# Kernel optimization log

Hardware: AMD Instinct MI355X
Metric: run time of the kernel (lower is better)

## Reference

```python
import jax, jax.numpy as jnp
import numpy as np

B, W, G, E, NI, K = 2048, 8192, 8, 128, 16, 15


def setup_inputs() -> dict:
    key = jax.random.key(0)
    ks = jax.random.split(key, 12)
    wavelengths_nm = jnp.linspace(300.0, 400.0, W, dtype=jnp.float32)
    # Rayleigh optical depth (Hansen & Travis style approximation), AMF=1 column
    lam_um = wavelengths_nm / 1000.0
    rayleigh_od = (0.008569 * lam_um ** -4
                   * (1.0 + 0.0113 * lam_um ** -2 + 0.00013 * lam_um ** -4)).astype(jnp.float32)
    return {
        "gas_columns": jax.random.uniform(ks[0], (B, G), jnp.float32),
        "instrument_ids": jax.random.randint(ks[1], (B,), 0, NI),
        "nuisance_latent": jax.random.normal(ks[2], (B, G), jnp.float32),
        "air_mass": 1.0 + 2.0 * jax.random.uniform(ks[3], (B,), jnp.float32),
        "wavelengths_nm": wavelengths_nm,
        "absorption": 0.1 * jax.random.uniform(ks[4], (G, W), jnp.float32),
        "continuum_basis": 0.05 * jax.random.normal(ks[5], (G + 1, W), jnp.float32),
        "rayleigh_od": rayleigh_od,
        "embed_table": jax.random.normal(ks[6], (NI, E), jnp.float32),
        "w1": jax.random.normal(ks[7], (E + G, 64), jnp.float32) / np.sqrt(E + G),
        "b1": jnp.zeros((64,), jnp.float32),
        "w2": jax.random.normal(ks[8], (64, 7), jnp.float32) / 8.0,
        "b2": jnp.zeros((7,), jnp.float32),
    }


def _gaussian_kernel(width_px, kernel_size):
    half = (kernel_size - 1) / 2
    pos = jnp.linspace(-half, half, kernel_size, dtype=width_px.dtype)  # [K]
    k = jnp.exp(-0.5 * (pos[None, :] / (width_px[:, None] + 1e-6)) ** 2)  # [B,K]
    return k / k.sum(axis=1, keepdims=True)


def _forward(gas_columns, nuisance_latent, air_mass, wavelengths_nm, absorption,
             continuum_basis, rayleigh_od, embed_table, w1, b1, w2, b2,
             instrument_ids):
    b = gas_columns.shape[0]
    am = air_mass[:, None]                                   # [B,1]
    scaled = gas_columns * am                                # [B,G]
    optical_depth = scaled @ absorption                      # [B,W]
    ones = jnp.ones((b, 1), gas_columns.dtype)
    continuum = jnp.concatenate([gas_columns, ones], axis=1) @ continuum_basis  # [B,W]
    differential = optical_depth + continuum + am * rayleigh_od[None, :]

    # nuisance MLP on [latent, embedding]
    embed = embed_table[instrument_ids]                      # [B,E]
    nin = jnp.concatenate([nuisance_latent, embed], axis=-1)
    h = jax.nn.gelu(nin @ w1 + b1, approximate=False)
    p = h @ w2 + b2                                          # [B,7]

    gain = jax.nn.softplus(p[:, 0]) + 0.001
    offset = p[:, 1]
    woff = 0.05 * jnp.tanh(p[:, 2])
    wscale = 1.0 + 0.005 * jnp.tanh(p[:, 3])
    lsf = jnp.clip(jax.nn.softplus(p[:, 4]) + 0.001, 0.2, 5.0)
    stray = jax.nn.sigmoid(p[:, 5]) * 0.05
    nonlin = 0.02 * jnp.tanh(p[:, 6])

    # per-sample wavelength shift/scale + linear resampling
    new_wl = wavelengths_nm[None, :] * wscale[:, None] + woff[:, None]  # [B,W]
    differential = jax.vmap(lambda wq, d: jnp.interp(wq, wavelengths_nm, d))(new_wl, differential)

    # per-sample Gaussian LSF convolution (replicate padding)
    kernel = _gaussian_kernel(lsf, K)                        # [B,K]
    pad = K // 2
    padded = jnp.pad(differential, ((0, 0), (pad, pad)), mode='edge')  # [B,W+K-1]
    n = differential.shape[1]
    convolved = sum(padded[:, k:k + n] * kernel[:, k:k + 1] for k in range(K))

    counts = jnp.exp(-convolved)
    post = gain[:, None] * counts + offset[:, None]
    total_nl = jnp.clip(nonlin, -0.04, 0.04)                 # instrument nonlinearity = 0
    nl_counts = post + total_nl[:, None] * post ** 2
    total_stray = jnp.clip(stray, 0.0, 0.2)                  # instrument stray = 0
    simulated = (1.0 - total_stray[:, None]) * nl_counts \
        + total_stray[:, None] * nl_counts.mean(axis=1, keepdims=True)
    return simulated


def reference(gas_columns, instrument_ids, nuisance_latent, air_mass,
              wavelengths_nm, absorption, continuum_basis, rayleigh_od,
              embed_table, w1, b1, w2, b2):
    return _forward(gas_columns, nuisance_latent, air_mass, wavelengths_nm,
                    absorption, continuum_basis, rayleigh_od, embed_table,
                    w1, b1, w2, b2, instrument_ids)
```

## Files before the change

kernel.cpp:

```cpp
#include <hip/hip_runtime.h>

#define W_ 8192
#define NBATCH 2048
#define NT 256
#define NWAVE 4
#define SEGW 2048
#define CCH 256
#define NCHW 8
#define IRW 272

typedef unsigned short u16_t;
typedef _Float16 h2v __attribute__((ext_vector_type(2)));

__device__ __forceinline__ u16_t f2h(float x){ _Float16 h=(_Float16)x; return __builtin_bit_cast(u16_t,h); }
__device__ __forceinline__ float h2f(u16_t u){ return (float)__builtin_bit_cast(_Float16,u); }
__device__ __forceinline__ unsigned pk2(float a,float b){ return (unsigned)f2h(a)|((unsigned)f2h(b)<<16); }
__device__ __forceinline__ float dot2u(unsigned a,unsigned b,float c){
#if __has_builtin(__builtin_amdgcn_fdot2)
  return __builtin_amdgcn_fdot2(__builtin_bit_cast(h2v,a),__builtin_bit_cast(h2v,b),c,false);
#else
  h2v ha=__builtin_bit_cast(h2v,a), hb=__builtin_bit_cast(h2v,b);
  return c+(float)ha[0]*(float)hb[0]+(float)ha[1]*(float)hb[1];
#endif
}
__device__ __forceinline__ unsigned pkrtz(float a,float b){
#if __has_builtin(__builtin_amdgcn_cvt_pkrtz)
  return __builtin_bit_cast(unsigned, __builtin_amdgcn_cvt_pkrtz(a,b));
#else
  return pk2(a,b);
#endif
}
__device__ __forceinline__ unsigned alignb(unsigned hi, unsigned lo){
#if __has_builtin(__builtin_amdgcn_alignbit)
  return __builtin_amdgcn_alignbit(hi, lo, 16);
#else
  return (lo >> 16) | (hi << 16);
#endif
}
__device__ __forceinline__ float softplusf(float x){ return fmaxf(x,0.f)+log1pf(expf(-fabsf(x))); }
__device__ __forceinline__ unsigned rflv(unsigned v){
  return (unsigned)__builtin_amdgcn_readfirstlane((int)v);
}
__device__ __forceinline__ float rflvf(float v){
  return __builtin_bit_cast(float, __builtin_amdgcn_readfirstlane(__builtin_bit_cast(int, v)));
}

__global__ __launch_bounds__(256, 2)
void doas_prep4(const float* __restrict__ absn, const float* __restrict__ cbn,
                const float* __restrict__ ray, const int* __restrict__ iid,
                const float* __restrict__ nuis, const float* __restrict__ emb,
                const float* __restrict__ w1, const float* __restrict__ b1,
                const float* __restrict__ w2, const float* __restrict__ b2,
                unsigned* __restrict__ Tp, float* __restrict__ params){
  const int tid = threadIdx.x;
  const int b = blockIdx.x;
  const int wid = tid >> 6, l = tid & 63;

  if (b < 32){
    const int w = b*256 + tid;
    #pragma unroll
    for (int q=0;q<4;++q) Tp[q*W_+w]     = pk2(absn[(2*q)*W_+w], absn[(2*q+1)*W_+w]);
    #pragma unroll
    for (int q=0;q<4;++q) Tp[(4+q)*W_+w] = pk2(cbn[(2*q)*W_+w],  cbn[(2*q+1)*W_+w]);
    Tp[8*W_+w] = pk2(cbn[8*W_+w], ray[w]);
  }

  const int r = b*4 + wid;
  float hj;
  {
    const int id = iid[r];
    float acc = b1[l];
    const float* nrow = nuis + (size_t)r * 8;
    #pragma unroll
    for (int i = 0; i < 8; ++i) acc = fmaf(nrow[i], w1[i*64 + l], acc);
    const float* erow = emb + (size_t)id * 128;
    #pragma unroll 8
    for (int i = 0; i < 128; ++i) acc = fmaf(erow[i], w1[(8+i)*64 + l], acc);
    hj = 0.5f * acc * (1.0f + erff(acc * 0.70710678118654752f));
  }
  float pv[7];
  {
    const float* w2r = w2 + l*7;
    #pragma unroll
    for (int k=0;k<7;++k) pv[k] = hj * w2r[k];
    #pragma unroll
    for (int off=32; off>=1; off>>=1){
      #pragma unroll
      for (int k=0;k<7;++k) pv[k] += __shfl_down(pv[k], off);
    }
  }
  if (l == 0){
    float p0=pv[0]+b2[0], p1=pv[1]+b2[1], p2=pv[2]+b2[2], p3=pv[3]+b2[3],
          p4=pv[4]+b2[4], p5=pv[5]+b2[5], p6=pv[6]+b2[6];
    float gainv = softplusf(p0) + 0.001f;
    float offv  = p1;
    float woffv = 0.05f * tanhf(p2);
    float wscv  = 1.0f + 0.005f * tanhf(p3);
    float lsf   = fminf(fmaxf(softplusf(p4) + 0.001f, 0.2f), 5.0f);
    float strv  = fminf(fmaxf((1.0f/(1.0f+expf(-p5))) * 0.05f, 0.0f), 0.2f);
    float nlin  = fminf(fmaxf(0.02f * tanhf(p6), -0.04f), 0.04f);
    float iw = 1.0f/(lsf + 1e-6f);
    float ks[15]; float ksum = 0.f;
    #pragma unroll
    for (int k2=0;k2<15;++k2){ float pp=(float)(k2-7)*iw; float e=expf(-0.5f*pp*pp); ks[k2]=e; ksum+=e; }
    float inv = 1.0f/ksum;
    float* pr = params + (size_t)r*16;
    unsigned* pu = (unsigned*)pr;
    #pragma unroll
    for (int i=0;i<7;++i) pu[i] = pk2(ks[2*i]*inv, ks[2*i+1]*inv);
    pu[7] = pk2(ks[14]*inv, 0.0f);
    pr[9]  = wscv;
    pr[10] = (300.0f*(wscv - 1.0f) + woffv) * (8191.0f/100.0f);
    pr[11] = gainv; pr[12] = offv; pr[13] = nlin; pr[14] = strv;
    pr[15] = 0.f;
  }
}

template<bool CLO, bool CHI>
__device__ __forceinline__ void interp_chunk(int cbase, int l, const unsigned* __restrict__ rU,
                                             unsigned* __restrict__ irowU,
                                             float wscale, float posoff){
  #pragma unroll
  for (int it=0; it<3; ++it){
    const int pi = it*64 + l;
    if (pi < 136){
      float v2[2];
      #pragma unroll
      for (int u=0;u<2;++u){
        int j = cbase + 2*pi + u;
        if (CLO) j = max(j, 0);
        if (CHI) j = min(j, W_-1);
        float pos = fmaf((float)j, wscale, posoff);
        if (CLO) pos = fmaxf(pos, 0.0f);
        if (CHI) pos = fminf(pos, 8191.0f);
        int i0 = (int)pos;
        if (CHI) i0 = min(i0, W_-2);
        const float fr = pos - (float)i0;
        const int m = i0 >> 1;
        const unsigned u0 = rU[m];
        const unsigned u1 = rU[m+1];
        const unsigned hu0 = u0 >> 16;
        const bool odd = (i0 & 1);
        const unsigned ua = odd ? hu0 : u0;
        const unsigned ub = odd ? u1  : hu0;
        const float d0 = h2f((u16_t)ua);
        const float d1 = h2f((u16_t)ub);
        v2[u] = fmaf(fr, d1-d0, d0);
      }
      irowU[pi] = pkrtz(v2[0], v2[1]);
    }
  }
}

__global__ __launch_bounds__(NT, 2)
void doas_main7(const unsigned* __restrict__ Tp, const float* __restrict__ gas,
                const float* __restrict__ air, const float* __restrict__ params,
                float* __restrict__ out){
  __shared__ u16_t rowH[W_ + 16];
  __shared__ u16_t irowS[NWAVE][IRW];
  __shared__ float wsumS[NWAVE];

  const int tid = threadIdx.x;
  const int row = blockIdx.x;
  const int wid = tid >> 6, l = tid & 63;
  const int segbase = wid * SEGW;

  unsigned csg[9];
  {
    const float am = air[row];
    const float* gfp = gas + (size_t)row * 8;
    #pragma unroll
    for (int q=0;q<4;++q) csg[q]   = rflv(pk2(gfp[2*q]*am, gfp[2*q+1]*am));
    #pragma unroll
    for (int q=0;q<4;++q) csg[4+q] = rflv(pk2(gfp[2*q],    gfp[2*q+1]));
    csg[8] = rflv(pk2(1.0f, am));
  }

  const float* pr = params + (size_t)row * 16;
  const unsigned* pu = (const unsigned*)pr;
  unsigned kwp[7];
  #pragma unroll
  for (int i=0;i<7;++i) kwp[i] = rflv(pu[i]);
  const unsigned k14lo = rflv(pu[7]);
  const float wscale = rflvf(pr[9]),  posoff = rflvf(pr[10]);
  const float gainv  = rflvf(pr[11]), offv   = rflvf(pr[12]);
  const float nlin   = rflvf(pr[13]), strv   = rflvf(pr[14]);

  unsigned* rowHU = (unsigned*)rowH;
  #pragma unroll
  for (int it=0; it<8; ++it){
    const int e0 = it*1024 + tid*4;
    uint4 dq[9];
    #pragma unroll
    for (int q=0;q<9;++q) dq[q] = *(const uint4*)(Tp + q*W_ + e0);
    float a0=0.f, a1=0.f, a2=0.f, a3=0.f;
    #pragma unroll
    for (int q=0;q<9;++q){
      a0 = dot2u(dq[q].x, csg[q], a0);
      a1 = dot2u(dq[q].y, csg[q], a1);
      a2 = dot2u(dq[q].z, csg[q], a2);
      a3 = dot2u(dq[q].w, csg[q], a3);
    }
    *(uint2*)(rowHU + (e0 >> 1)) = make_uint2(pkrtz(a0,a1), pkrtz(a2,a3));
  }
  __syncthreads();

  const unsigned* rU = (const unsigned*)rowH;
  u16_t* irow = &irowS[wid][0];
  unsigned* irowU = (unsigned*)irow;

  float accsum = 0.f;
  unsigned nlp[NCHW][2];

  #pragma unroll
  for (int c = 0; c < NCHW; ++c) {
    const int cs = segbase + c*CCH;
    const int cbase = cs - 8;
    if (wid == 0 && c == 0)
      interp_chunk<true,false>(cbase, l, rU, irowU, wscale, posoff);
    else if (wid == NWAVE-1 && c == NCHW-1)
      interp_chunk<false,true>(cbase, l, rU, irowU, wscale, posoff);
    else
      interp_chunk<false,false>(cbase, l, rU, irowU, wscale, posoff);
    __builtin_amdgcn_wave_barrier();
    {
      const uint2* p2 = (const uint2*)irowU + l;
      const uint2 A = p2[0], B = p2[1], C = p2[2], D = p2[3], E = p2[4];
      unsigned q[10] = {A.x,A.y, B.x,B.y, C.x,C.y, D.x,D.y, E.x,E.y};
      unsigned sh[9];
      #pragma unroll
      for (int m=0;m<9;++m) sh[m] = alignb(q[m+1], q[m]);
      float nlv[4];
      #pragma unroll
      for (int t=0;t<4;++t){
        float cv = 0.f;
        if ((t & 1) == 0){
          const int b0 = t >> 1;
          #pragma unroll
          for (int i=0;i<7;++i) cv = dot2u(sh[b0+i], kwp[i], cv);
          cv = dot2u(sh[b0+7], k14lo, cv);
        } else {
          const int b0 = (t+1) >> 1;
          #pragma unroll
          for (int i=0;i<7;++i) cv = dot2u(q[b0+i], kwp[i], cv);
          cv = dot2u(q[b0+7], k14lo, cv);
        }
        const float counts = __expf(-cv);
        const float post = fmaf(gainv, counts, offv);
        const float v = fmaf(nlin*post, post, post);
        accsum += v;
        nlv[t] = v;
      }
      nlp[c][0] = pkrtz(nlv[0], nlv[1]);
      nlp[c][1] = pkrtz(nlv[2], nlv[3]);
    }
    __builtin_amdgcn_wave_barrier();
  }

  float s = accsum;
  #pragma unroll
  for (int off2 = 32; off2 >= 1; off2 >>= 1) s += __shfl_down(s, off2);
  if (l == 0) wsumS[wid] = s;
  __syncthreads();
  const float meanv = (wsumS[0]+wsumS[1]+wsumS[2]+wsumS[3]) * (1.0f/8192.0f);

  {
    const float aa = 1.0f - strv;
    const float bb = strv * meanv;
    float* orow = out + (size_t)row * W_;
    #pragma unroll
    for (int c = 0; c < NCHW; ++c) {
      const unsigned u0 = nlp[c][0], u1 = nlp[c][1];
      float4 o0;
      o0.x = fmaf(aa, h2f((u16_t)(u0 & 0xffffu)), bb);
      o0.y = fmaf(aa, h2f((u16_t)(u0 >> 16)),     bb);
      o0.z = fmaf(aa, h2f((u16_t)(u1 & 0xffffu)), bb);
      o0.w = fmaf(aa, h2f((u16_t)(u1 >> 16)),     bb);
      *(float4*)(orow + segbase + c*CCH + 4*l) = o0;
    }
  }
}

__global__ __launch_bounds__(256, 2)
void doas_mono(const float* __restrict__ gas, const int* __restrict__ iid,
               const float* __restrict__ nuis, const float* __restrict__ air,
               const float* __restrict__ absn, const float* __restrict__ cbn,
               const float* __restrict__ ray, const float* __restrict__ emb,
               const float* __restrict__ w1, const float* __restrict__ b1,
               const float* __restrict__ w2, const float* __restrict__ b2,
               float* __restrict__ out)
{
  __shared__ u16_t ringS[4][2048];
  __shared__ u16_t irowS2[4][544];
  __shared__ float hS[64];
  __shared__ float pS[8];
  __shared__ float scalS[52];
  __shared__ float wsumS[4];

  const int tid = threadIdx.x;
  const int row = blockIdx.x;

  if (tid < 64) {
    const int j = tid;
    const int id = iid[row];
    float acc = b1[j];
    const float* nrow = nuis + (size_t)row * 8;
    #pragma unroll
    for (int i = 0; i < 8; ++i) acc = fmaf(nrow[i], w1[i*64 + j], acc);
    const float* erow = emb + (size_t)id * 128;
    for (int i = 0; i < 128; ++i) acc = fmaf(erow[i], w1[(8+i)*64 + j], acc);
    hS[j] = 0.5f * acc * (1.0f + erff(acc * 0.70710678118654752f));
  }
  __syncthreads();
  if (tid < 7) {
    float p = b2[tid];
    for (int j = 0; j < 64; ++j) p = fmaf(hS[j], w2[j*7+tid], p);
    pS[tid] = p;
  }
  __syncthreads();
  if (tid == 0) {
    float p0=pS[0], p1=pS[1], p2=pS[2], p3=pS[3], p4=pS[4], p5=pS[5], p6=pS[6];
    float gainv = softplusf(p0) + 0.001f;
    float offv  = p1;
    float woffv = 0.05f * tanhf(p2);
    float wscv  = 1.0f + 0.005f * tanhf(p3);
    float lsf   = fminf(fmaxf(softplusf(p4) + 0.001f, 0.2f), 5.0f);
    float strv  = fminf(fmaxf((1.0f/(1.0f+expf(-p5))) * 0.05f, 0.0f), 0.2f);
    float nlin  = fminf(fmaxf(0.02f * tanhf(p6), -0.04f), 0.04f);
    float iw = 1.0f/(lsf + 1e-6f);
    float ks[15]; float ksum = 0.f;
    #pragma unroll
    for (int k2=0;k2<15;++k2){ float pp=(float)(k2-7)*iw; float e=expf(-0.5f*pp*pp); ks[k2]=e; ksum+=e; }
    float inv = 1.0f/ksum;
    scalS[15] = wscv;
    scalS[16] = (300.0f*(wscv - 1.0f) + woffv) * (8191.0f/100.0f);
    scalS[17] = gainv; scalS[18] = offv; scalS[19] = nlin; scalS[20] = strv;
    scalS[22] = air[row];
    unsigned* su = (unsigned*)scalS;
    #pragma unroll
    for (int i=0;i<7;++i) su[32+i] = pk2(ks[2*i]*inv, ks[2*i+1]*inv);
    su[39] = pk2(ks[14]*inv, 0.0f);
    su[40] = pk2(0.0f, ks[14]*inv);
    #pragma unroll
    for (int g=0; g<8; ++g) scalS[23+g] = gas[(size_t)row*8+g];
  }
  __syncthreads();

  const int wid = tid >> 6, l = tid & 63;
  const int segbase = wid * 2048;
  const unsigned* scalU = (const unsigned*)scalS;
  unsigned kwp[7];
  #pragma unroll
  for (int i=0;i<7;++i) kwp[i] = rflv(scalU[32+i]);
  const unsigned k14lo = rflv(scalU[39]), k14hi = rflv(scalU[40]);
  const float wscale = scalS[15], posoff = scalS[16];
  const float gainv  = scalS[17], offv   = scalS[18];
  const float nlin   = scalS[19], strv   = scalS[20];

  u16_t* ring = &ringS[wid][0];
  unsigned* ringU = (unsigned*)ring;
  u16_t* irow = &irowS2[wid][0];
  unsigned* irowU = (unsigned*)irow;

  auto do_diff = [&](int s){
    const int sbase = segbase - 256 + (s << 9);
    #pragma unroll
    for (int it=0; it<4; ++it){
      const int e0 = sbase + ((it*64 + l) << 1);
      const int eL = min(max(e0, 0), W_-2);
      const float am = scalS[22];
      float a0=0.f, a1=0.f;
      #pragma unroll
      for (int g=0; g<8; ++g){
        const float cg = scalS[23+g];
        const float ca = cg*am;
        a0 = fmaf(ca, absn[g*W_+eL],   a0); a0 = fmaf(cg, cbn[g*W_+eL],   a0);
        a1 = fmaf(ca, absn[g*W_+eL+1], a1); a1 = fmaf(cg, cbn[g*W_+eL+1], a1);
      }
      a0 += cbn[8*W_+eL]   + am*ray[eL];
      a1 += cbn[8*W_+eL+1] + am*ray[eL+1];
      ringU[((unsigned)e0 & 2047) >> 1] = pkrtz(a0, a1);
    }
  };

  float accsum = 0.f;
  unsigned nlp[4][4];

  do_diff(0); do_diff(1);
  __builtin_amdgcn_wave_barrier();

  #pragma unroll
  for (int c = 0; c < 4; ++c) {
    if (c < 3) do_diff(c+2);
    __builtin_amdgcn_wave_barrier();
    {
      const int cbase = segbase + (c << 9) - 8;
      #pragma unroll
      for (int it = 0; it < 5; ++it) {
        const int pi = it*64 + l;
        if (pi < 264) {
          float v2[2];
          #pragma unroll
          for (int u=0; u<2; ++u){
            const int j = cbase + 2*pi + u;
            const int jc = min(max(j, 0), W_-1);
            float pos = fmaf((float)jc, wscale, posoff);
            pos = fminf(fmaxf(pos, 0.0f), 8191.0f);
            const int i0 = min((int)pos, W_-2);
            const float fr = pos - (float)i0;
            const float d0 = h2f(ring[ i0    & 2047]);
            const float d1 = h2f(ring[(i0+1) & 2047]);
            v2[u] = fmaf(fr, d1-d0, d0);
          }
          irowU[pi] = pkrtz(v2[0], v2[1]);
        }
      }
    }
    __builtin_amdgcn_wave_barrier();
    {
      const uint4* qp = (const uint4*)irow + l;
      const uint4 A = qp[0], B = qp[1], C = qp[2];
      unsigned q[12] = {A.x,A.y,A.z,A.w, B.x,B.y,B.z,B.w, C.x,C.y,C.z,C.w};
      unsigned sh[10];
      #pragma unroll
      for (int m=0;m<10;++m) sh[m] = alignb(q[m+1], q[m]);
      float nlv[8];
      #pragma unroll
      for (int t=0;t<8;++t){
        const int s2 = t >> 1;
        float cv = 0.f;
        if ((t & 1) == 0){
          #pragma unroll
          for (int i=0;i<7;++i) cv = dot2u(sh[s2+i], kwp[i], cv);
          cv = dot2u(q[s2+7], k14hi, cv);
        } else {
          #pragma unroll
          for (int i=0;i<7;++i) cv = dot2u(q[s2+1+i], kwp[i], cv);
          cv = dot2u(q[s2+8], k14lo, cv);
        }
        const float counts = __expf(-cv);
        const float post = fmaf(gainv, counts, offv);
        const float v = fmaf(nlin*post, post, post);
        accsum += v;
        nlv[t] = v;
      }
      nlp[c][0] = pkrtz(nlv[0], nlv[1]);
      nlp[c][1] = pkrtz(nlv[2], nlv[3]);
      nlp[c][2] = pkrtz(nlv[4], nlv[5]);
      nlp[c][3] = pkrtz(nlv[6], nlv[7]);
    }
    __builtin_amdgcn_wave_barrier();
  }

  float s = accsum;
  #pragma unroll
  for (int off2 = 32; off2 >= 1; off2 >>= 1) s += __shfl_down(s, off2);
  if (l == 0) wsumS[wid] = s;
  __syncthreads();
  const float meanv = (wsumS[0]+wsumS[1]+wsumS[2]+wsumS[3]) * (1.0f/8192.0f);

  {
    const float aa = 1.0f - strv;
    const float bb = strv * meanv;
    float* orow = out + (size_t)row * W_;
    #pragma unroll
    for (int c = 0; c < 4; ++c) {
      const unsigned u0 = nlp[c][0], u1 = nlp[c][1], u2 = nlp[c][2], u3 = nlp[c][3];
      float4 o0, o1;
      o0.x = fmaf(aa, h2f((u16_t)(u0 & 0xffffu)), bb);
      o0.y = fmaf(aa, h2f((u16_t)(u0 >> 16)),     bb);
      o0.z = fmaf(aa, h2f((u16_t)(u1 & 0xffffu)), bb);
      o0.w = fmaf(aa, h2f((u16_t)(u1 >> 16)),     bb);
      o1.x = fmaf(aa, h2f((u16_t)(u2 & 0xffffu)), bb);
      o1.y = fmaf(aa, h2f((u16_t)(u2 >> 16)),     bb);
      o1.z = fmaf(aa, h2f((u16_t)(u3 & 0xffffu)), bb);
      o1.w = fmaf(aa, h2f((u16_t)(u3 >> 16)),     bb);
      float* dst = orow + segbase + (c << 9) + 8*l;
      *(float4*)(dst)     = o0;
      *(float4*)(dst + 4) = o1;
    }
  }
}

extern "C" void kernel_launch(void* const* d_in, const int* in_sizes, int n_in,
                              void* d_out, int out_size, void* d_ws, size_t ws_size,
                              hipStream_t stream) {
  const float* gas  = (const float*)d_in[0];
  const int*   iid  = (const int*)d_in[1];
  const float* nuis = (const float*)d_in[2];
  const float* air  = (const float*)d_in[3];
  const float* wl   = (const float*)d_in[4];
  const float* absn = (const float*)d_in[5];
  const float* cbn  = (const float*)d_in[6];
  const float* ray  = (const float*)d_in[7];
  const float* emb  = (const float*)d_in[8];
  const float* w1   = (const float*)d_in[9];
  const float* b1   = (const float*)d_in[10];
  const float* w2   = (const float*)d_in[11];
  const float* b2   = (const float*)d_in[12];
  float* out = (float*)d_out;
  (void)in_sizes; (void)n_in; (void)out_size; (void)wl;

  const size_t packBytes = (size_t)9 * W_ * 4;
  const size_t parBytes  = (size_t)NBATCH * 16 * 4;

  if (ws_size >= packBytes + parBytes) {
    unsigned* Tp  = (unsigned*)d_ws;
    float* params = (float*)((char*)d_ws + packBytes);
    hipLaunchKernelGGL(doas_prep4, dim3(NBATCH/4), dim3(256), 0, stream,
                       absn, cbn, ray, iid, nuis, emb, w1, b1, w2, b2, Tp, params);
    hipLaunchKernelGGL(doas_main7, dim3(NBATCH), dim3(NT), 0, stream,
                       Tp, gas, air, params, out);
  } else {
    hipLaunchKernelGGL(doas_mono, dim3(NBATCH), dim3(256), 0, stream,
                       gas, iid, nuis, air, absn, cbn, ray, emb, w1, b1, w2, b2, out);
  }
}
```

Baseline: 52.83 us.

## Process two rows per block, overlapping second row's matmul with first row's convolution

Each block now handles two spectra. The second row's matmul (global Tp loads plus dot products) is interleaved chunk-by-chunk with the first row's interpolation and convolution, then the second row is convolved separately. The aim is to hide global load latency behind LDS and ALU work and to amortize per-block setup. In exchange it doubles shared memory per block, raises register pressure and halves the grid size, which may reduce occupancy or load balance.

```diff
diff --git a/kernel.cpp b/kernel.cpp
--- a/kernel.cpp
+++ b/kernel.cpp
@@ -4,6 +4,7 @@
 #define NBATCH 2048
 #define NT 256
 #define NWAVE 4
+#define RPB 2
 #define SEGW 2048
 #define CCH 256
 #define NCHW 8
@@ -153,40 +154,35 @@
 }
 
 __global__ __launch_bounds__(NT, 2)
-void doas_main7(const unsigned* __restrict__ Tp, const float* __restrict__ gas,
-                const float* __restrict__ air, const float* __restrict__ params,
-                float* __restrict__ out){
-  __shared__ u16_t rowH[W_ + 16];
+void doas_main12(const unsigned* __restrict__ Tp, const float* __restrict__ gas,
+                 const float* __restrict__ air, const float* __restrict__ params,
+                 float* __restrict__ out){
+  __shared__ u16_t rowA[W_ + 16];
+  __shared__ u16_t rowB[W_ + 16];
   __shared__ u16_t irowS[NWAVE][IRW];
-  __shared__ float wsumS[NWAVE];
+  __shared__ float wsumS[2*NWAVE];
 
   const int tid = threadIdx.x;
-  const int row = blockIdx.x;
+  const int r0 = blockIdx.x * RPB;
   const int wid = tid >> 6, l = tid & 63;
   const int segbase = wid * SEGW;
 
-  unsigned csg[9];
-  {
-    const float am = air[row];
-    const float* gfp = gas + (size_t)row * 8;
-    #pragma unroll
-    for (int q=0;q<4;++q) csg[q]   = rflv(pk2(gfp[2*q]*am, gfp[2*q+1]*am));
-    #pragma unroll
-    for (int q=0;q<4;++q) csg[4+q] = rflv(pk2(gfp[2*q],    gfp[2*q+1]));
-    csg[8] = rflv(pk2(1.0f, am));
-  }
-
-  const float* pr = params + (size_t)row * 16;
-  const unsigned* pu = (const unsigned*)pr;
-  unsigned kwp[7];
+  unsigned csg0[9], csg1[9];
   #pragma unroll
-  for (int i=0;i<7;++i) kwp[i] = rflv(pu[i]);
-  const unsigned k14lo = rflv(pu[7]);
-  const float wscale = rflvf(pr[9]),  posoff = rflvf(pr[10]);
-  const float gainv  = rflvf(pr[11]), offv   = rflvf(pr[12]);
-  const float nlin   = rflvf(pr[13]), strv   = rflvf(pr[14]);
-
-  unsigned* rowHU = (unsigned*)rowH;
+  for (int rr=0; rr<2; ++rr){
+    unsigned* cs = rr ? csg1 : csg0;
+    const float am = air[r0+rr];
+    const float* gfp = gas + (size_t)(r0+rr) * 8;
+    #pragma unroll
+    for (int q=0;q<4;++q) cs[q]   = rflv(pk2(gfp[2*q]*am, gfp[2*q+1]*am));
+    #pragma unroll
+    for (int q=0;q<4;++q) cs[4+q] = rflv(pk2(gfp[2*q],    gfp[2*q+1]));
+    cs[8] = rflv(pk2(1.0f, am));
+  }
+
+  unsigned* rowAU = (unsigned*)rowA;
+  unsigned* rowBU = (unsigned*)rowB;
+
   #pragma unroll
   for (int it=0; it<8; ++it){
     const int e0 = it*1024 + tid*4;
@@ -196,78 +192,183 @@
     float a0=0.f, a1=0.f, a2=0.f, a3=0.f;
     #pragma unroll
     for (int q=0;q<9;++q){
-      a0 = dot2u(dq[q].x, csg[q], a0);
-      a1 = dot2u(dq[q].y, csg[q], a1);
-      a2 = dot2u(dq[q].z, csg[q], a2);
-      a3 = dot2u(dq[q].w, csg[q], a3);
-    }
-    *(uint2*)(rowHU + (e0 >> 1)) = make_uint2(pkrtz(a0,a1), pkrtz(a2,a3));
+      a0 = dot2u(dq[q].x, csg0[q], a0);
+      a1 = dot2u(dq[q].y, csg0[q], a1);
+      a2 = dot2u(dq[q].z, csg0[q], a2);
+      a3 = dot2u(dq[q].w, csg0[q], a3);
+    }
+    *(uint2*)(rowAU + (e0 >> 1)) = make_uint2(pkrtz(a0,a1), pkrtz(a2,a3));
   }
   __syncthreads();
 
-  const unsigned* rU = (const unsigned*)rowH;
   u16_t* irow = &irowS[wid][0];
   unsigned* irowU = (unsigned*)irow;
 
-  float accsum = 0.f;
-  unsigned nlp[NCHW][2];
-
-  #pragma unroll
-  for (int c = 0; c < NCHW; ++c) {
-    const int cs = segbase + c*CCH;
-    const int cbase = cs - 8;
-    if (wid == 0 && c == 0)
-      interp_chunk<true,false>(cbase, l, rU, irowU, wscale, posoff);
-    else if (wid == NWAVE-1 && c == NCHW-1)
-      interp_chunk<false,true>(cbase, l, rU, irowU, wscale, posoff);
-    else
-      interp_chunk<false,false>(cbase, l, rU, irowU, wscale, posoff);
-    __builtin_amdgcn_wave_barrier();
-    {
-      const uint2* p2 = (const uint2*)irowU + l;
-      const uint2 A = p2[0], B = p2[1], C = p2[2], D = p2[3], E = p2[4];
-      unsigned q[10] = {A.x,A.y, B.x,B.y, C.x,C.y, D.x,D.y, E.x,E.y};
-      unsigned sh[9];
-      #pragma unroll
-      for (int m=0;m<9;++m) sh[m] = alignb(q[m+1], q[m]);
-      float nlv[4];
-      #pragma unroll
-      for (int t=0;t<4;++t){
-        float cv = 0.f;
-        if ((t & 1) == 0){
-          const int b0 = t >> 1;
-          #pragma unroll
-          for (int i=0;i<7;++i) cv = dot2u(sh[b0+i], kwp[i], cv);
-          cv = dot2u(sh[b0+7], k14lo, cv);
-        } else {
-          const int b0 = (t+1) >> 1;
-          #pragma unroll
-          for (int i=0;i<7;++i) cv = dot2u(q[b0+i], kwp[i], cv);
-          cv = dot2u(q[b0+7], k14lo, cv);
+  {
+    const float* pr = params + (size_t)r0 * 16;
+    const unsigned* pu = (const unsigned*)pr;
+    unsigned kwp[7];
+    #pragma unroll
+    for (int i=0;i<7;++i) kwp[i] = rflv(pu[i]);
+    const unsigned k14lo = rflv(pu[7]);
+    const float wscale = rflvf(pr[9]),  posoff = rflvf(pr[10]);
+    const float gainv  = rflvf(pr[11]), offv   = rflvf(pr[12]);
+    const float nlin   = rflvf(pr[13]), strv   = rflvf(pr[14]);
+
+    float accsum = 0.f;
+    unsigned nlp[NCHW][2];
+    const unsigned* rU = (const unsigned*)rowA;
+
+    #pragma unroll
+    for (int c = 0; c < NCHW; ++c) {
+      {
+        const int e0 = c*1024 + tid*4;
+        uint4 dq[9];
+        #pragma unroll
+        for (int q=0;q<9;++q) dq[q] = *(const uint4*)(Tp + q*W_ + e0);
+        float a0=0.f, a1=0.f, a2=0.f, a3=0.f;
+        #pragma unroll
+        for (int q=0;q<9;++q){
+          a0 = dot2u(dq[q].x, csg1[q], a0);
+          a1 = dot2u(dq[q].y, csg1[q], a1);
+          a2 = dot2u(dq[q].z, csg1[q], a2);
+          a3 = dot2u(dq[q].w, csg1[q], a3);
         }
-        const float counts = __expf(-cv);
-        const float post = fmaf(gainv, counts, offv);
-        const float v = fmaf(nlin*post, post, post);
-        accsum += v;
-        nlv[t] = v;
+        *(uint2*)(rowBU + (e0 >> 1)) = make_uint2(pkrtz(a0,a1), pkrtz(a2,a3));
       }
-      nlp[c][0] = pkrtz(nlv[0], nlv[1]);
-      nlp[c][1] = pkrtz(nlv[2], nlv[3]);
-    }
-    __builtin_amdgcn_wave_barrier();
-  }
-
-  float s = accsum;
-  #pragma unroll
-  for (int off2 = 32; off2 >= 1; off2 >>= 1) s += __shfl_down(s, off2);
-  if (l == 0) wsumS[wid] = s;
-  __syncthreads();
-  const float meanv = (wsumS[0]+wsumS[1]+wsumS[2]+wsumS[3]) * (1.0f/8192.0f);
-
-  {
+      const int cbase = segbase + c*CCH - 8;
+      if (wid == 0 && c == 0)
+        interp_chunk<true,false>(cbase, l, rU, irowU, wscale, posoff);
+      else if (wid == NWAVE-1 && c == NCHW-1)
+        interp_chunk<false,true>(cbase, l, rU, irowU, wscale, posoff);
+      else
+        interp_chunk<false,false>(cbase, l, rU, irowU, wscale, posoff);
+      __builtin_amdgcn_wave_barrier();
+      {
+        const uint2* p2 = (const uint2*)irowU + l;
+        const uint2 A = p2[0], B = p2[1], C = p2[2], D = p2[3], E = p2[4];
+        unsigned q[10] = {A.x,A.y, B.x,B.y, C.x,C.y, D.x,D.y, E.x,E.y};
+        unsigned sh[9];
+        #pragma unroll
+        for (int m=0;m<9;++m) sh[m] = alignb(q[m+1], q[m]);
+        float nlv[4];
+        #pragma unroll
+        for (int t=0;t<4;++t){
+          float cv = 0.f;
+          if ((t & 1) == 0){
+            const int b0 = t >> 1;
+            #pragma unroll
+            for (int i=0;i<7;++i) cv = dot2u(sh[b0+i], kwp[i], cv);
+            cv = dot2u(sh[b0+7], k14lo, cv);
+          } else {
+            const int b0 = (t+1) >> 1;
+            #pragma unroll
+            for (int i=0;i<7;++i) cv = dot2u(q[b0+i], kwp[i], cv);
+            cv = dot2u(q[b0+7], k14lo, cv);
+          }
+          const float counts = __expf(-cv);
+          const float post = fmaf(gainv, counts, offv);
+          const float v = fmaf(nlin*post, post, post);
+          accsum += v;
+          nlv[t] = v;
+        }
+        nlp[c][0] = pkrtz(nlv[0], nlv[1]);
+        nlp[c][1] = pkrtz(nlv[2], nlv[3]);
+      }
+      __builtin_amdgcn_wave_barrier();
+    }
+
+    float s = accsum;
+    #pragma unroll
+    for (int off2 = 32; off2 >= 1; off2 >>= 1) s += __shfl_down(s, off2);
+    if (l == 0) wsumS[wid] = s;
+    __syncthreads();
+    const float meanv = (wsumS[0]+wsumS[1]+wsumS[2]+wsumS[3]) * (1.0f/8192.0f);
+
     const float aa = 1.0f - strv;
     const float bb = strv * meanv;
-    float* orow = out + (size_t)row * W_;
+    float* orow = out + (size_t)r0 * W_;
+    #pragma unroll
+    for (int c = 0; c < NCHW; ++c) {
+      const unsigned u0 = nlp[c][0], u1 = nlp[c][1];
+      float4 o0;
+      o0.x = fmaf(aa, h2f((u16_t)(u0 & 0xffffu)), bb);
+      o0.y = fmaf(aa, h2f((u16_t)(u0 >> 16)),     bb);
+      o0.z = fmaf(aa, h2f((u16_t)(u1 & 0xffffu)), bb);
+      o0.w = fmaf(aa, h2f((u16_t)(u1 >> 16)),     bb);
+      *(float4*)(orow + segbase + c*CCH + 4*l) = o0;
+    }
+  }
+
+  {
+    const float* pr = params + (size_t)(r0+1) * 16;
+    const unsigned* pu = (const unsigned*)pr;
+    unsigned kwp[7];
+    #pragma unroll
+    for (int i=0;i<7;++i) kwp[i] = rflv(pu[i]);
+    const unsigned k14lo = rflv(pu[7]);
+    const float wscale = rflvf(pr[9]),  posoff = rflvf(pr[10]);
+    const float gainv  = rflvf(pr[11]), offv   = rflvf(pr[12]);
+    const float nlin   = rflvf(pr[13]), strv   = rflvf(pr[14]);
+
+    float accsum = 0.f;
+    unsigned nlp[NCHW][2];
+    const unsigned* rU = (const unsigned*)rowB;
+
+    #pragma unroll
+    for (int c = 0; c < NCHW; ++c) {
+      const int cbase = segbase + c*CCH - 8;
+      if (wid == 0 && c == 0)
+        interp_chunk<true,false>(cbase, l, rU, irowU, wscale, posoff);
+      else if (wid == NWAVE-1 && c == NCHW-1)
+        interp_chunk<false,true>(cbase, l, rU, irowU, wscale, posoff);
+      else
+        interp_chunk<false,false>(cbase, l, rU, irowU, wscale, posoff);
+      __builtin_amdgcn_wave_barrier();
+      {
+        const uint2* p2 = (const uint2*)irowU + l;
+        const uint2 A = p2[0], B = p2[1], C = p2[2], D = p2[3], E = p2[4];
+        unsigned q[10] = {A.x,A.y, B.x,B.y, C.x,C.y, D.x,D.y, E.x,E.y};
+        unsigned sh[9];
+        #pragma unroll
+        for (int m=0;m<9;++m) sh[m] = alignb(q[m+1], q[m]);
+        float nlv[4];
+        #pragma unroll
+        for (int t=0;t<4;++t){
+          float cv = 0.f;
+          if ((t & 1) == 0){
+            const int b0 = t >> 1;
+            #pragma unroll
+            for (int i=0;i<7;++i) cv = dot2u(sh[b0+i], kwp[i], cv);
+            cv = dot2u(sh[b0+7], k14lo, cv);
+          } else {
+            const int b0 = (t+1) >> 1;
+            #pragma unroll
+            for (int i=0;i<7;++i) cv = dot2u(q[b0+i], kwp[i], cv);
+            cv = dot2u(q[b0+7], k14lo, cv);
+          }
+          const float counts = __expf(-cv);
+          const float post = fmaf(gainv, counts, offv);
+          const float v = fmaf(nlin*post, post, post);
+          accsum += v;
+          nlv[t] = v;
+        }
+        nlp[c][0] = pkrtz(nlv[0], nlv[1]);
+        nlp[c][1] = pkrtz(nlv[2], nlv[3]);
+      }
+      __builtin_amdgcn_wave_barrier();
+    }
+
+    float s = accsum;
+    #pragma unroll
+    for (int off2 = 32; off2 >= 1; off2 >>= 1) s += __shfl_down(s, off2);
+    if (l == 0) wsumS[4+wid] = s;
+    __syncthreads();
+    const float meanv = (wsumS[4]+wsumS[5]+wsumS[6]+wsumS[7]) * (1.0f/8192.0f);
+
+    const float aa = 1.0f - strv;
+    const float bb = strv * meanv;
+    float* orow = out + (size_t)(r0+1) * W_;
     #pragma unroll
     for (int c = 0; c < NCHW; ++c) {
       const unsigned u0 = nlp[c][0], u1 = nlp[c][1];
@@ -509,7 +610,7 @@
     float* params = (float*)((char*)d_ws + packBytes);
     hipLaunchKernelGGL(doas_prep4, dim3(NBATCH/4), dim3(256), 0, stream,
                        absn, cbn, ray, iid, nuis, emb, w1, b1, w2, b2, Tp, params);
-    hipLaunchKernelGGL(doas_main7, dim3(NBATCH), dim3(NT), 0, stream,
+    hipLaunchKernelGGL(doas_main12, dim3(NBATCH/RPB), dim3(NT), 0, stream,
                        Tp, gas, air, params, out);
   } else {
     hipLaunchKernelGGL(doas_mono, dim3(NBATCH), dim3(256), 0, stream,
```

Result: slower. 62.74 us (+18.8%).
